# Performance work log

Measured on AMD Instinct MI355X. Metric: run time of the kernel, lower is better.

## Reference

```python
import math
import jax, jax.numpy as jnp
import numpy as np

B, S, H, NH = 2, 1536, 2048, 16
DH = H // NH  # 128
FP16_MIN = float(jnp.finfo(jnp.float16).min)


def setup_inputs() -> dict:
    key = jax.random.key(0)
    ks = jax.random.split(key, 6)
    std = 0.02
    return {
        "x": jax.random.normal(ks[0], (B, S, H), dtype=jnp.float32),
        "attention_bias": jax.random.normal(ks[1], (B, NH, S, S), dtype=jnp.float32),
        "Wq": jax.random.normal(ks[2], (H, H), dtype=jnp.float32) * std,
        "Wk": jax.random.normal(ks[3], (H, H), dtype=jnp.float32) * std,
        "Wv": jax.random.normal(ks[4], (H, H), dtype=jnp.float32) * std,
        "Wo": jax.random.normal(ks[5], (H, H), dtype=jnp.float32) * std,
    }


def reference(x, attention_bias, Wq, Wk, Wv, Wo):
    b, s, h = x.shape
    # QKV projections (nn.Linear with bias=False: y = x @ W.T)
    q = (x @ Wq.T).reshape(b, s, NH, DH).transpose(0, 2, 1, 3)  # b h s d
    k = (x @ Wk.T).reshape(b, s, NH, DH).transpose(0, 2, 1, 3)
    v = (x @ Wv.T).reshape(b, s, NH, DH).transpose(0, 2, 1, 3)
    # bias[:, :, -s:, -s:] is identity here since bias is already [b,h,s,s]
    bias = attention_bias[:, :, -s:, -s:]
    # mask where tril(bias) == 0 (upper triangle and any exact zeros in lower)
    masked = jnp.tril(bias) == 0
    bias = jnp.where(masked, FP16_MIN, bias)
    # torch SDPA default scale = 1/sqrt(head_dim) (module's softmax_scale unused)
    scale = 1.0 / math.sqrt(DH)
    scores = jnp.einsum("bhqd,bhkd->bhqk", q, k) * scale + bias
    attn = jax.nn.softmax(scores, axis=-1)
    out = jnp.einsum("bhqk,bhkd->bhqd", attn, v)  # b h s d
    out = out.transpose(0, 2, 1, 3).reshape(b, s, h)  # b s (h d)
    return out @ Wo.T
```

## Files before the change

kernel.cpp:

```cpp
#include <hip/hip_runtime.h>
#include <cstdint>
#include <stddef.h>

typedef short short8 __attribute__((ext_vector_type(8)));
typedef float floatx4 __attribute__((ext_vector_type(4)));
typedef unsigned short ushortx4 __attribute__((ext_vector_type(4)));

#define MFMA16(a, b, c) __builtin_amdgcn_mfma_f32_16x16x32_bf16((a), (b), (c), 0, 0, 0)

static constexpr int Bv = 2, Sv = 1536, Hv = 2048, NHv = 16, DHv = 128;
static constexpr int Mv = Bv * Sv;
static constexpr float SCALE = 0.08838834764831845f;

__device__ inline unsigned short f2bf(float f) {
  union { float f; unsigned u; } c; c.f = f;
  unsigned u = c.u;
  u += 0x7fffu + ((u >> 16) & 1u);
  return (unsigned short)(u >> 16);
}

__device__ inline void async_copy16(const void* g, void* l) {
  auto gp = reinterpret_cast<__attribute__((address_space(1))) uint32_t*>(
      reinterpret_cast<uintptr_t>(g));
  auto lp = reinterpret_cast<__attribute__((address_space(3))) uint32_t*>(
      reinterpret_cast<uintptr_t>(l));
  __builtin_amdgcn_global_load_lds(gp, lp, 16, 0, 0);
}

__global__ void cvt_all_kernel(const float* __restrict__ x,
    const float* __restrict__ Wq, const float* __restrict__ Wk,
    const float* __restrict__ Wv, const float* __restrict__ Wo,
    unsigned short* __restrict__ xb, unsigned short* __restrict__ wqb,
    unsigned short* __restrict__ wkb, unsigned short* __restrict__ wvb,
    unsigned short* __restrict__ wob) {
  const int i = blockIdx.x * 256 + threadIdx.x;
  const int nx4 = (Mv * Hv) / 4;
  const float* src; unsigned short* dst; int j; float scl = 1.0f;
  if (i < nx4) {
    src = x; dst = xb; j = i;
  } else {
    const int i2 = i - nx4;
    const int wsel = i2 >> 20;
    j = i2 & ((1 << 20) - 1);
    if (wsel == 0)      { src = Wq; dst = wqb; scl = SCALE; }
    else if (wsel == 1) { src = Wk; dst = wkb; }
    else if (wsel == 2) { src = Wv; dst = wvb; }
    else                { src = Wo; dst = wob; }
  }
  const float4 v = reinterpret_cast<const float4*>(src)[j];
  ushortx4 o;
  o[0] = f2bf(v.x * scl); o[1] = f2bf(v.y * scl);
  o[2] = f2bf(v.z * scl); o[3] = f2bf(v.w * scl);
  reinterpret_cast<ushortx4*>(dst)[j] = o;
}

template <int TM, bool WF32>
__global__ __launch_bounds__(256) void gemm_bt_kernel(
    const unsigned short* __restrict__ A,
    const unsigned short* __restrict__ W0, const unsigned short* __restrict__ W1,
    const unsigned short* __restrict__ W2,
    void* __restrict__ C0, void* __restrict__ C1, void* __restrict__ C2) {
  constexpr int MI = TM / 32;
  __shared__ __align__(16) unsigned short As[TM * 64];
  __shared__ __align__(16) unsigned short Bs[128 * 64];
  const int z = blockIdx.z;
  const unsigned short* W = (z == 0) ? W0 : ((z == 1) ? W1 : W2);
  const int tid = threadIdx.x;
  const int w = tid >> 6, lane = tid & 63;
  const int quad = lane >> 4, l15 = lane & 15;
  const int wr = w >> 1, wc = w & 1;
  const int tileM = blockIdx.y * TM, tileN = blockIdx.x * 128;

  floatx4 acc[MI][4];
#pragma unroll
  for (int i = 0; i < MI; ++i)
#pragma unroll
    for (int j = 0; j < 4; ++j)
#pragma unroll
      for (int r = 0; r < 4; ++r) acc[i][j][r] = 0.0f;

  size_t aoff[MI]; int alb[MI];
#pragma unroll
  for (int m = 0; m < MI; ++m) {
    const int slot = m * 256 + tid;
    const int row = slot >> 3, blk = slot & 7;
    aoff[m] = (size_t)(tileM + row) * 2048 + ((blk ^ (row & 7)) * 8);
    alb[m] = (m * 256 + w * 64) * 8;
  }
  size_t boff[4]; int blb[4];
#pragma unroll
  for (int m = 0; m < 4; ++m) {
    const int slot = m * 256 + tid;
    const int row = slot >> 3, blk = slot & 7;
    boff[m] = (size_t)(tileN + row) * 2048 + ((blk ^ (row & 7)) * 8);
    blb[m] = (m * 256 + w * 64) * 8;
  }

  for (int k0 = 0; k0 < 2048; k0 += 64) {
    __syncthreads();
#pragma unroll
    for (int m = 0; m < MI; ++m) async_copy16(A + aoff[m] + k0, As + alb[m]);
#pragma unroll
    for (int m = 0; m < 4; ++m) async_copy16(W + boff[m] + k0, Bs + blb[m]);
    __syncthreads();
#pragma unroll
    for (int kk = 0; kk < 2; ++kk) {
      const int swz = (((kk * 4 + quad) ^ (l15 & 7)) * 8);
      short8 af[MI], bfr[4];
#pragma unroll
      for (int i = 0; i < MI; ++i)
        af[i] = *(const short8*)(As + (wr * (TM / 2) + i * 16 + l15) * 64 + swz);
#pragma unroll
      for (int j = 0; j < 4; ++j)
        bfr[j] = *(const short8*)(Bs + (wc * 64 + j * 16 + l15) * 64 + swz);
#pragma unroll
      for (int i = 0; i < MI; ++i)
#pragma unroll
        for (int j = 0; j < 4; ++j) acc[i][j] = MFMA16(af[i], bfr[j], acc[i][j]);
    }
  }

  void* C = (z == 0) ? C0 : ((z == 1) ? C1 : C2);
#pragma unroll
  for (int i = 0; i < MI; ++i) {
#pragma unroll
    for (int r = 0; r < 4; ++r) {
      const int row = tileM + wr * (TM / 2) + i * 16 + quad * 4 + r;
#pragma unroll
      for (int j = 0; j < 4; ++j) {
        const int col = tileN + wc * 64 + j * 16 + l15;
        if (WF32)
          ((float*)C)[(size_t)row * 2048 + col] = acc[i][j][r];
        else
          ((unsigned short*)C)[(size_t)row * 2048 + col] = f2bf(acc[i][j][r]);
      }
    }
  }
}

__global__ __launch_bounds__(256) void vtrans_kernel(
    const unsigned short* __restrict__ V, unsigned short* __restrict__ Vtg) {
  __shared__ unsigned short Vs[64 * 132];
  const int t0 = blockIdx.x * 64, h = blockIdx.y, b = blockIdx.z;
  const int tid = threadIdx.x;
  const int w = tid >> 6, lane = tid & 63;
#pragma unroll
  for (int m = 0; m < 4; ++m) {
    const int idx = m * 256 + tid;
    const int tr = idx >> 4, blk = idx & 15;
    const unsigned short* src = V + ((size_t)(b * Sv) + t0 + tr) * Hv + h * DHv + blk * 8;
    ushortx4 v0 = *(const ushortx4*)(src);
    ushortx4 v1 = *(const ushortx4*)(src + 4);
    *(ushortx4*)(Vs + tr * 132 + blk * 8) = v0;
    *(ushortx4*)(Vs + tr * 132 + blk * 8 + 4) = v1;
  }
  __syncthreads();
  const size_t obase = ((size_t)(b * NHv + h) * DHv) * Sv + t0;
#pragma unroll 4
  for (int p = 0; p < 32; ++p) {
    const int d = p * 4 + w;
    Vtg[obase + (size_t)d * Sv + lane] = Vs[lane * 132 + d];
  }
}

__global__ __launch_bounds__(256) void attn_kernel(
    const unsigned short* __restrict__ Qg, const unsigned short* __restrict__ Kg,
    const unsigned short* __restrict__ Vtg, const float* __restrict__ bias,
    unsigned short* __restrict__ Og) {
  __shared__ __align__(16) unsigned short Ks[64 * 128];
  __shared__ __align__(16) unsigned short Vt[128 * 64];
  __shared__ __align__(16) unsigned short Ps[4 * 16 * 64];

  const int xb = blockIdx.x;
  const int qt = (xb & 1) ? (23 - (xb >> 1)) : (xb >> 1);
  const int h = blockIdx.y, b = blockIdx.z;
  const int q0 = qt * 64;
  const int tid = threadIdx.x;
  const int w = tid >> 6, lane = tid & 63;
  const int quad = lane >> 4, l15 = lane & 15;

  const size_t bh_base = (size_t)(b * Sv) * Hv + (size_t)h * DHv;
  const size_t vt_base = ((size_t)(b * NHv + h) * DHv) * Sv;

  short8 qf[4];
  {
    const unsigned short* qbase = Qg + bh_base + (size_t)(q0 + w * 16 + l15) * Hv;
#pragma unroll
    for (int kk = 0; kk < 4; ++kk)
      qf[kk] = *(const short8*)(qbase + kk * 32 + quad * 8);
  }

  floatx4 o[8];
#pragma unroll
  for (int n = 0; n < 8; ++n)
#pragma unroll
    for (int r = 0; r < 4; ++r) o[n][r] = 0.0f;
  float lrow[4] = {0.0f, 0.0f, 0.0f, 0.0f};

  const float* biasbase = bias + (size_t)(b * NHv + h) * Sv * Sv;
  unsigned short* pw = Ps + w * 1024;

  size_t koff[4], voff[4]; int lbs[4];
#pragma unroll
  for (int m = 0; m < 4; ++m) {
    const int sK = m * 256 + tid;
    const int rK = sK >> 4, bK = sK & 15;
    koff[m] = bh_base + (size_t)rK * Hv + ((bK ^ (rK & 15)) * 8);
    const int sV = m * 256 + tid;
    const int rV = sV >> 3, bV = sV & 7;
    voff[m] = vt_base + (size_t)rV * Sv + ((bV ^ (rV & 7)) * 8);
    lbs[m] = (m * 256 + w * 64) * 8;
  }

  float bv[4][4];
#pragma unroll
  for (int r = 0; r < 4; ++r) {
    const size_t brow = (size_t)(q0 + w * 16 + quad * 4 + r) * Sv;
#pragma unroll
    for (int j = 0; j < 4; ++j) bv[r][j] = biasbase[brow + j * 16 + l15];
  }

  for (int kt = 0; kt <= qt; ++kt) {
    const int k0 = kt * 64;
    __syncthreads();
#pragma unroll
    for (int m = 0; m < 4; ++m) {
      async_copy16(Kg + koff[m] + (size_t)k0 * Hv, Ks + lbs[m]);
      async_copy16(Vtg + voff[m] + k0, Vt + lbs[m]);
    }
    __syncthreads();

    const int kn = (kt < qt) ? k0 + 64 : k0;
    float bvn[4][4];
#pragma unroll
    for (int r = 0; r < 4; ++r) {
      const size_t brow = (size_t)(q0 + w * 16 + quad * 4 + r) * Sv;
#pragma unroll
      for (int j = 0; j < 4; ++j) bvn[r][j] = biasbase[brow + kn + j * 16 + l15];
    }

    floatx4 sacc[4];
#pragma unroll
    for (int j = 0; j < 4; ++j) {
#pragma unroll
      for (int r = 0; r < 4; ++r) sacc[j][r] = 0.0f;
      const int kr = j * 16 + l15;
#pragma unroll
      for (int kk = 0; kk < 4; ++kk) {
        const int g = kk * 4 + quad;
        short8 bfrag = *(const short8*)(Ks + kr * 128 + (g ^ (kr & 15)) * 8);
        sacc[j] = MFMA16(qf[kk], bfrag, sacc[j]);
      }
    }

    const bool diag = (kt == qt);
#pragma unroll
    for (int r = 0; r < 4; ++r) {
      const int qrow = q0 + w * 16 + quad * 4 + r;
      const int prow = quad * 4 + r;
      float acc_l = 0.0f;
#pragma unroll
      for (int j = 0; j < 4; ++j) {
        const int col = j * 16 + l15;
        float p = __expf(sacc[j][r] + bv[r][j]);
        if (diag && (k0 + col) > qrow) p = 0.0f;
        acc_l += p;
        pw[prow * 64 + ((col >> 3) ^ (prow & 7)) * 8 + (col & 7)] = f2bf(p);
      }
      lrow[r] += acc_l;
    }
#pragma unroll
    for (int r = 0; r < 4; ++r)
#pragma unroll
      for (int j = 0; j < 4; ++j) bv[r][j] = bvn[r][j];

#pragma unroll
    for (int kk = 0; kk < 2; ++kk) {
      const int g = kk * 4 + quad;
      short8 pa = *(const short8*)(pw + l15 * 64 + (g ^ (l15 & 7)) * 8);
#pragma unroll
      for (int n = 0; n < 8; ++n) {
        const int dr = n * 16 + l15;
        short8 vbf = *(const short8*)(Vt + dr * 64 + (g ^ (dr & 7)) * 8);
        o[n] = MFMA16(pa, vbf, o[n]);
      }
    }
  }

#pragma unroll
  for (int r = 0; r < 4; ++r) {
    float ls = lrow[r];
#pragma unroll
    for (int off = 1; off < 16; off <<= 1) ls += __shfl_xor(ls, off, 64);
    const float inv = 1.0f / ls;
    const int qrow = q0 + w * 16 + quad * 4 + r;
    const size_t rowbase = bh_base + (size_t)qrow * Hv;
#pragma unroll
    for (int n = 0; n < 8; ++n)
      Og[rowbase + n * 16 + l15] = f2bf(o[n][r] * inv);
  }
}

extern "C" void kernel_launch(void* const* d_in, const int* in_sizes, int n_in,
                              void* d_out, int out_size, void* d_ws, size_t ws_size,
                              hipStream_t stream) {
  const float* x = (const float*)d_in[0];
  const float* bias = (const float*)d_in[1];
  const float* Wq = (const float*)d_in[2];
  const float* Wk = (const float*)d_in[3];
  const float* Wv = (const float*)d_in[4];
  const float* Wo = (const float*)d_in[5];
  float* out = (float*)d_out;

  unsigned short* xb = (unsigned short*)d_ws;
  unsigned short* wqb = xb + (size_t)Mv * Hv;
  unsigned short* wkb = wqb + (size_t)Hv * Hv;
  unsigned short* wvb = wkb + (size_t)Hv * Hv;
  unsigned short* wob = wvb + (size_t)Hv * Hv;
  unsigned short* qb = wob + (size_t)Hv * Hv;
  unsigned short* kb = qb + (size_t)Mv * Hv;
  unsigned short* vb = kb + (size_t)Mv * Hv;
  unsigned short* ob = vb + (size_t)Mv * Hv;
  unsigned short* vtb = xb;
  const size_t needed = ((size_t)Mv * Hv * 5 + (size_t)Hv * Hv * 4) * 2;
  if (ws_size < needed) return;

  const int cvt_n = (Mv * Hv) / 4 + Hv * Hv;
  cvt_all_kernel<<<dim3(cvt_n / 256), 256, 0, stream>>>(
      x, Wq, Wk, Wv, Wo, xb, wqb, wkb, wvb, wob);

  gemm_bt_kernel<128, false><<<dim3(16, 24, 3), 256, 0, stream>>>(
      xb, wqb, wkb, wvb, qb, kb, vb);

  vtrans_kernel<<<dim3(24, 16, 2), 256, 0, stream>>>(vb, vtb);

  attn_kernel<<<dim3(24, NHv, Bv), 256, 0, stream>>>(qb, kb, vtb, bias, ob);

  gemm_bt_kernel<64, true><<<dim3(16, 48, 1), 256, 0, stream>>>(
      ob, wob, wob, wob, out, out, out);
}
```

Before: 625.8 us.

## Fuse V transpose into QKV GEMM epilogue and drop LDS staging in attention

The QKV GEMM now writes V directly in transposed per-head layout from its epilogue, which removes the separate transpose kernel and its extra pass over V. The attention kernel stops staging K and V^T tiles through shared memory with block-wide barriers. Each wave instead loads its MFMA fragments for K and V^T straight from global memory (relying on cache), and launch bounds request 3 blocks per CU. This trades shared-memory reuse across the four waves of a block for fewer barriers and lower LDS use, at the risk of more global/L2 traffic and less coalesced, strided loads for V^T.

Measured after the change: 800.5 us. 1.28x slower.

```diff
diff --git a/kernel.cpp b/kernel.cpp
--- a/kernel.cpp
+++ b/kernel.cpp
@@ -54,7 +54,7 @@
   reinterpret_cast<ushortx4*>(dst)[j] = o;
 }
 
-template <int TM, bool WF32>
+template <int TM, bool WF32, bool VT>
 __global__ __launch_bounds__(256) void gemm_bt_kernel(
     const unsigned short* __restrict__ A,
     const unsigned short* __restrict__ W0, const unsigned short* __restrict__ W1,
@@ -120,6 +120,27 @@
     }
   }
 
+  if (VT && z == 2) {
+    unsigned short* Vt = (unsigned short*)C2;
+    const int bb = (tileM >= Sv) ? 1 : 0;
+    const int tokb = tileM - bb * Sv;
+    const int hh = blockIdx.x;
+    const size_t hbase = (size_t)(bb * NHv + hh) * DHv;
+#pragma unroll
+    for (int i = 0; i < MI; ++i) {
+      const int tok = tokb + wr * (TM / 2) + i * 16 + quad * 4;
+#pragma unroll
+      for (int j = 0; j < 4; ++j) {
+        const int d = wc * 64 + j * 16 + l15;
+        ushortx4 pk;
+#pragma unroll
+        for (int r = 0; r < 4; ++r) pk[r] = f2bf(acc[i][j][r]);
+        *(ushortx4*)(Vt + (hbase + d) * Sv + tok) = pk;
+      }
+    }
+    return;
+  }
+
   void* C = (z == 0) ? C0 : ((z == 1) ? C1 : C2);
 #pragma unroll
   for (int i = 0; i < MI; ++i) {
@@ -138,53 +159,28 @@
   }
 }
 
-__global__ __launch_bounds__(256) void vtrans_kernel(
-    const unsigned short* __restrict__ V, unsigned short* __restrict__ Vtg) {
-  __shared__ unsigned short Vs[64 * 132];
-  const int t0 = blockIdx.x * 64, h = blockIdx.y, b = blockIdx.z;
-  const int tid = threadIdx.x;
-  const int w = tid >> 6, lane = tid & 63;
-#pragma unroll
-  for (int m = 0; m < 4; ++m) {
-    const int idx = m * 256 + tid;
-    const int tr = idx >> 4, blk = idx & 15;
-    const unsigned short* src = V + ((size_t)(b * Sv) + t0 + tr) * Hv + h * DHv + blk * 8;
-    ushortx4 v0 = *(const ushortx4*)(src);
-    ushortx4 v1 = *(const ushortx4*)(src + 4);
-    *(ushortx4*)(Vs + tr * 132 + blk * 8) = v0;
-    *(ushortx4*)(Vs + tr * 132 + blk * 8 + 4) = v1;
-  }
-  __syncthreads();
-  const size_t obase = ((size_t)(b * NHv + h) * DHv) * Sv + t0;
-#pragma unroll 4
-  for (int p = 0; p < 32; ++p) {
-    const int d = p * 4 + w;
-    Vtg[obase + (size_t)d * Sv + lane] = Vs[lane * 132 + d];
-  }
-}
-
-__global__ __launch_bounds__(256) void attn_kernel(
+__global__ __launch_bounds__(256, 3) void attn_kernel(
     const unsigned short* __restrict__ Qg, const unsigned short* __restrict__ Kg,
     const unsigned short* __restrict__ Vtg, const float* __restrict__ bias,
     unsigned short* __restrict__ Og) {
-  __shared__ __align__(16) unsigned short Ks[64 * 128];
-  __shared__ __align__(16) unsigned short Vt[128 * 64];
   __shared__ __align__(16) unsigned short Ps[4 * 16 * 64];
 
   const int xb = blockIdx.x;
   const int qt = (xb & 1) ? (23 - (xb >> 1)) : (xb >> 1);
   const int h = blockIdx.y, b = blockIdx.z;
-  const int q0 = qt * 64;
   const int tid = threadIdx.x;
   const int w = tid >> 6, lane = tid & 63;
   const int quad = lane >> 4, l15 = lane & 15;
+  const int q0 = qt * 64 + w * 16;
 
   const size_t bh_base = (size_t)(b * Sv) * Hv + (size_t)h * DHv;
-  const size_t vt_base = ((size_t)(b * NHv + h) * DHv) * Sv;
+  const size_t vt_base = (size_t)(b * NHv + h) * DHv * Sv;
+  const float* biasbase = bias + (size_t)(b * NHv + h) * Sv * Sv;
+  unsigned short* pw = Ps + w * 1024;
 
   short8 qf[4];
   {
-    const unsigned short* qbase = Qg + bh_base + (size_t)(q0 + w * 16 + l15) * Hv;
+    const unsigned short* qbase = Qg + bh_base + (size_t)(q0 + l15) * Hv;
 #pragma unroll
     for (int kk = 0; kk < 4; ++kk)
       qf[kk] = *(const short8*)(qbase + kk * 32 + quad * 8);
@@ -197,44 +193,33 @@
     for (int r = 0; r < 4; ++r) o[n][r] = 0.0f;
   float lrow[4] = {0.0f, 0.0f, 0.0f, 0.0f};
 
-  const float* biasbase = bias + (size_t)(b * NHv + h) * Sv * Sv;
-  unsigned short* pw = Ps + w * 1024;
-
-  size_t koff[4], voff[4]; int lbs[4];
-#pragma unroll
-  for (int m = 0; m < 4; ++m) {
-    const int sK = m * 256 + tid;
-    const int rK = sK >> 4, bK = sK & 15;
-    koff[m] = bh_base + (size_t)rK * Hv + ((bK ^ (rK & 15)) * 8);
-    const int sV = m * 256 + tid;
-    const int rV = sV >> 3, bV = sV & 7;
-    voff[m] = vt_base + (size_t)rV * Sv + ((bV ^ (rV & 7)) * 8);
-    lbs[m] = (m * 256 + w * 64) * 8;
-  }
-
   float bv[4][4];
 #pragma unroll
   for (int r = 0; r < 4; ++r) {
-    const size_t brow = (size_t)(q0 + w * 16 + quad * 4 + r) * Sv;
+    const size_t brow = (size_t)(q0 + quad * 4 + r) * Sv;
 #pragma unroll
     for (int j = 0; j < 4; ++j) bv[r][j] = biasbase[brow + j * 16 + l15];
   }
+
+  const unsigned short* kbase = Kg + bh_base;
 
   for (int kt = 0; kt <= qt; ++kt) {
     const int k0 = kt * 64;
-    __syncthreads();
-#pragma unroll
-    for (int m = 0; m < 4; ++m) {
-      async_copy16(Kg + koff[m] + (size_t)k0 * Hv, Ks + lbs[m]);
-      async_copy16(Vtg + voff[m] + k0, Vt + lbs[m]);
-    }
-    __syncthreads();
+
+    short8 kf[4][4];
+#pragma unroll
+    for (int j = 0; j < 4; ++j) {
+      const unsigned short* kr = kbase + (size_t)(k0 + j * 16 + l15) * Hv + quad * 8;
+#pragma unroll
+      for (int kk = 0; kk < 4; ++kk)
+        kf[j][kk] = *(const short8*)(kr + kk * 32);
+    }
 
     const int kn = (kt < qt) ? k0 + 64 : k0;
     float bvn[4][4];
 #pragma unroll
     for (int r = 0; r < 4; ++r) {
-      const size_t brow = (size_t)(q0 + w * 16 + quad * 4 + r) * Sv;
+      const size_t brow = (size_t)(q0 + quad * 4 + r) * Sv;
 #pragma unroll
       for (int j = 0; j < 4; ++j) bvn[r][j] = biasbase[brow + kn + j * 16 + l15];
     }
@@ -244,19 +229,15 @@
     for (int j = 0; j < 4; ++j) {
 #pragma unroll
       for (int r = 0; r < 4; ++r) sacc[j][r] = 0.0f;
-      const int kr = j * 16 + l15;
-#pragma unroll
-      for (int kk = 0; kk < 4; ++kk) {
-        const int g = kk * 4 + quad;
-        short8 bfrag = *(const short8*)(Ks + kr * 128 + (g ^ (kr & 15)) * 8);
-        sacc[j] = MFMA16(qf[kk], bfrag, sacc[j]);
-      }
+#pragma unroll
+      for (int kk = 0; kk < 4; ++kk)
+        sacc[j] = MFMA16(qf[kk], kf[j][kk], sacc[j]);
     }
 
     const bool diag = (kt == qt);
 #pragma unroll
     for (int r = 0; r < 4; ++r) {
-      const int qrow = q0 + w * 16 + quad * 4 + r;
+      const int qrow = q0 + quad * 4 + r;
       const int prow = quad * 4 + r;
       float acc_l = 0.0f;
 #pragma unroll
@@ -278,11 +259,11 @@
     for (int kk = 0; kk < 2; ++kk) {
       const int g = kk * 4 + quad;
       short8 pa = *(const short8*)(pw + l15 * 64 + (g ^ (l15 & 7)) * 8);
+      const unsigned short* vr = Vtg + vt_base + (size_t)l15 * Sv + k0 + kk * 32 + quad * 8;
 #pragma unroll
       for (int n = 0; n < 8; ++n) {
-        const int dr = n * 16 + l15;
-        short8 vbf = *(const short8*)(Vt + dr * 64 + (g ^ (dr & 7)) * 8);
-        o[n] = MFMA16(pa, vbf, o[n]);
+        short8 vf = *(const short8*)(vr + (size_t)n * 16 * Sv);
+        o[n] = MFMA16(pa, vf, o[n]);
       }
     }
   }
@@ -293,8 +274,7 @@
 #pragma unroll
     for (int off = 1; off < 16; off <<= 1) ls += __shfl_xor(ls, off, 64);
     const float inv = 1.0f / ls;
-    const int qrow = q0 + w * 16 + quad * 4 + r;
-    const size_t rowbase = bh_base + (size_t)qrow * Hv;
+    const size_t rowbase = bh_base + (size_t)(q0 + quad * 4 + r) * Hv;
 #pragma unroll
     for (int n = 0; n < 8; ++n)
       Og[rowbase + n * 16 + l15] = f2bf(o[n][r] * inv);
@@ -319,9 +299,8 @@
   unsigned short* wob = wvb + (size_t)Hv * Hv;
   unsigned short* qb = wob + (size_t)Hv * Hv;
   unsigned short* kb = qb + (size_t)Mv * Hv;
-  unsigned short* vb = kb + (size_t)Mv * Hv;
-  unsigned short* ob = vb + (size_t)Mv * Hv;
-  unsigned short* vtb = xb;
+  unsigned short* vtb = kb + (size_t)Mv * Hv;
+  unsigned short* ob = vtb + (size_t)Mv * Hv;
   const size_t needed = ((size_t)Mv * Hv * 5 + (size_t)Hv * Hv * 4) * 2;
   if (ws_size < needed) return;
 
@@ -329,13 +308,11 @@
   cvt_all_kernel<<<dim3(cvt_n / 256), 256, 0, stream>>>(
       x, Wq, Wk, Wv, Wo, xb, wqb, wkb, wvb, wob);
 
-  gemm_bt_kernel<128, false><<<dim3(16, 24, 3), 256, 0, stream>>>(
-      xb, wqb, wkb, wvb, qb, kb, vb);
-
-  vtrans_kernel<<<dim3(24, 16, 2), 256, 0, stream>>>(vb, vtb);
+  gemm_bt_kernel<128, false, true><<<dim3(16, 24, 3), 256, 0, stream>>>(
+      xb, wqb, wkb, wvb, qb, kb, vtb);
 
   attn_kernel<<<dim3(24, NHv, Bv), 256, 0, stream>>>(qb, kb, vtb, bias, ob);
 
-  gemm_bt_kernel<64, true><<<dim3(16, 48, 1), 256, 0, stream>>>(
+  gemm_bt_kernel<64, true, false><<<dim3(16, 48, 1), 256, 0, stream>>>(
       ob, wob, wob, wob, out, out, out);
 }
```
